# Performance work log

Measured on AMD Instinct MI355X. Metric: run time of the kernel, lower is better.

The kernel has to match this reference:

```python
import jax, jax.numpy as jnp
import numpy as np

HIDDEN = 768
VOCAB = 30522
PAD_IDX = 0


def setup_inputs() -> dict:
    key = jax.random.key(0)
    ks = jax.random.split(key, 12)
    B, J, X, D, V, K = 32, 4, 256, HIDDEN, VOCAB, 8
    s = 0.02
    return {
        "decoder_input": jax.random.normal(ks[0], (B, J, D), jnp.float32),
        "hidden": jax.random.normal(ks[1], (1, B, D), jnp.float32),
        "encoder_output": jax.random.normal(ks[2], (B, X, D), jnp.float32),
        "input_ids": jax.random.randint(ks[3], (B, X), 0, V),
        "max_len": K,
        "emb": jax.random.normal(ks[4], (V, D), jnp.float32) * s,
        "w_ih": jax.random.normal(ks[5], (3 * D, D), jnp.float32) * s,
        "w_hh": jax.random.normal(ks[6], (3 * D, D), jnp.float32) * s,
        "b_ih": jnp.zeros((3 * D,), jnp.float32),
        "b_hh": jnp.zeros((3 * D,), jnp.float32),
        "w_gen": jax.random.normal(ks[7], (1, 3 * D), jnp.float32) * s,
        "b_gen": jnp.zeros((1,), jnp.float32),
    }


def _gru_cell(x, h, w_ih, w_hh, b_ih, b_hh):
    # PyTorch GRUCell math. x,h: (B,D)
    gi = x @ w_ih.T + b_ih  # (B,3D)
    gh = h @ w_hh.T + b_hh
    i_r, i_z, i_n = jnp.split(gi, 3, axis=-1)
    h_r, h_z, h_n = jnp.split(gh, 3, axis=-1)
    r = jax.nn.sigmoid(i_r + h_r)
    z = jax.nn.sigmoid(i_z + h_z)
    n = jnp.tanh(i_n + r * h_n)
    return (1.0 - z) * n + z * h


def _decode(decoder_input, hidden, encoder_output, input_ids, max_len,
            emb, w_ih, w_hh, b_ih, b_hh, w_gen, b_gen):
    B = input_ids.shape[0]
    V = emb.shape[0]
    mask = input_ids == PAD_IDX  # (B,X)
    rows = jnp.arange(B)[:, None]
    h0 = hidden[0]  # (B,D)

    def step(carry, _):
        x, h = carry  # (B,D), (B,D)
        h = _gru_cell(x, h, w_ih, w_hh, b_ih, b_hh)
        # vocab distribution
        p_vcb = jax.nn.softmax(h @ emb.T, axis=-1)  # (B,V)
        # context attention
        attn_ctx = jnp.einsum("bxd,bd->bx", encoder_output, h)
        attn_ctx = jnp.where(mask, -1e9, attn_ctx)
        attn_ctx = jax.nn.softmax(attn_ctx, axis=-1)  # (B,X)
        context = jnp.einsum("bx,bxd->bd", attn_ctx, encoder_output)
        # pointer-generator gate
        p_gen = jax.nn.sigmoid(
            jnp.concatenate([h, x, context], axis=-1) @ w_gen.T + b_gen
        )  # (B,1)
        # scatter copy probs into vocab space
        p_ctx = jnp.zeros((B, V), attn_ctx.dtype).at[rows, input_ids].add(attn_ctx)
        p_svg = p_gen * p_vcb + (1.0 - p_gen) * p_ctx  # (B,V)
        x_next = emb[jnp.argmax(p_svg, axis=-1)]  # greedy next input (B,D)
        return (x_next, h), p_svg

    outs = []
    h = h0
    for j in range(decoder_input.shape[1]):  # small fixed J'
        (_, h), p = jax.lax.scan(step, (decoder_input[:, j, :], h), None,
                                 length=max_len)
        outs.append(jnp.transpose(p, (1, 0, 2)))  # (B,K,V)
    return jnp.stack(outs, axis=1)  # (B,J',K,V)


def reference(decoder_input, hidden, encoder_output, input_ids, max_len,
              emb, w_ih, w_hh, b_ih, b_hh, w_gen, b_gen):
    return _decode(decoder_input, hidden, encoder_output, input_ids, max_len,
                   emb, w_ih, w_hh, b_ih, b_hh, w_gen, b_gen)
```

## Files before the change

### kernel.cpp

```cpp
#include <hip/hip_runtime.h>
#include <hip/hip_bf16.h>

#define D 768
#define BB 32
#define XX 256
#define CH 3816
#define NLG 128

typedef __bf16 bf16x8 __attribute__((ext_vector_type(8)));
typedef float  f32x4  __attribute__((ext_vector_type(4)));

__global__ __launch_bounds__(256) void k_cvt(const float* __restrict__ src,
                                             __bf16* __restrict__ dst, int n8)
{
    int i = blockIdx.x * 256 + threadIdx.x;
    if (i < n8) {
        float4 f0 = *(const float4*)(src + (size_t)i * 8);
        float4 f1 = *(const float4*)(src + (size_t)i * 8 + 4);
        bf16x8 o;
        o[0] = (__bf16)f0.x; o[1] = (__bf16)f0.y; o[2] = (__bf16)f0.z; o[3] = (__bf16)f0.w;
        o[4] = (__bf16)f1.x; o[5] = (__bf16)f1.y; o[6] = (__bf16)f1.z; o[7] = (__bf16)f1.w;
        *(bf16x8*)(dst + (size_t)i * 8) = o;
    }
}

__global__ __launch_bounds__(256) void k_penc(
    const float* __restrict__ enc, const float* __restrict__ wgen,
    float* __restrict__ penc)
{
    const int t = threadIdx.x;
    const int b = blockIdx.x >> 2, c = blockIdx.x & 3;
    const int x0 = c * 64;
    const int l = t & 31;
    float4 wr[6];
    #pragma unroll
    for (int p = 0; p < 6; ++p)
        wr[p] = *(const float4*)(wgen + 1536 + l * 4 + p * 128);
    for (int g = 0; g < 8; ++g) {
        int x = x0 + g * 8 + (t >> 5);
        const float* er = enc + ((size_t)b * XX + x) * D + l * 4;
        float acc = 0.f;
        #pragma unroll
        for (int p = 0; p < 6; ++p) {
            float4 e = *(const float4*)(er + p * 128);
            acc += e.x * wr[p].x + e.y * wr[p].y + e.z * wr[p].z + e.w * wr[p].w;
        }
        #pragma unroll
        for (int m = 1; m <= 16; m <<= 1) acc += __shfl_xor(acc, m);
        if (l == 0) penc[b * XX + x] = acc;
    }
}

__global__ __launch_bounds__(256) void k_gates(
    const float* __restrict__ xbase, long xbstride,
    const unsigned long long* __restrict__ toks,
    const float* __restrict__ hin,
    const float* __restrict__ wih, const float* __restrict__ whh,
    float* __restrict__ gT)
{
    __shared__ __align__(16) float vec[BB][132];
    __shared__ int tokl[BB];
    const int t = threadIdx.x, bid = blockIdx.x;
    const int b = t & 31, rl = t >> 5;
    const int rglob = bid * 8 + rl;
    const bool isH = rglob >= 2304;
    const int row = isH ? rglob - 2304 : rglob;
    const float* w = (isH ? whh : wih) + (size_t)row * D;
    if (t < 32) tokl[t] = toks ? (int)(0xFFFFFFFFu - (unsigned)(toks[t] & 0xFFFFFFFFull)) : 0;

    float acc = 0.f;
    for (int c = 0; c < 6; ++c) {
        const int kc = c * 128;
        __syncthreads();
        for (int p = 0; p < 4; ++p) {
            int fid = t + 256 * p;
            int bb = fid >> 5, k4 = (fid & 31) * 4;
            const float* src;
            if (isH) src = hin + (size_t)bb * D;
            else     src = toks ? (xbase + (size_t)tokl[bb] * D)
                                : (xbase + (size_t)bb * xbstride);
            *(float4*)&vec[bb][k4] = *(const float4*)(src + kc + k4);
        }
        __syncthreads();
        #pragma unroll
        for (int k4 = 0; k4 < 128; k4 += 4) {
            float4 wv = *(const float4*)(w + kc + k4);
            float4 xv = *(const float4*)&vec[b][k4];
            acc += wv.x * xv.x + wv.y * xv.y + wv.z * xv.z + wv.w * xv.w;
        }
    }
    gT[(size_t)rglob * 32 + b] = acc;
}

__global__ __launch_bounds__(256) void k_comb(
    const float* __restrict__ gT,
    const float* __restrict__ bih, const float* __restrict__ bhh,
    const float* __restrict__ hin,
    const float* __restrict__ xbase, long xbstride,
    const unsigned long long* __restrict__ toks,
    const float* __restrict__ wgen,
    float* __restrict__ hout, __bf16* __restrict__ hbf,
    float* __restrict__ pgen_part,
    unsigned long long* __restrict__ argz)
{
    __shared__ float part[8][32];
    const int t = threadIdx.x, bid = blockIdx.x;
    const int b = t & 31, dl = t >> 5;
    const int d = bid * 8 + dl;
    if (bid == 0 && t < 32) argz[t] = 0ULL;
    float ir = gT[(size_t)d * 32 + b]            + bih[d];
    float iz = gT[(size_t)(768 + d) * 32 + b]    + bih[768 + d];
    float in_ = gT[(size_t)(1536 + d) * 32 + b]  + bih[1536 + d];
    float hr = gT[(size_t)(2304 + d) * 32 + b]   + bhh[d];
    float hz = gT[(size_t)(3072 + d) * 32 + b]   + bhh[768 + d];
    float hn = gT[(size_t)(3840 + d) * 32 + b]   + bhh[1536 + d];
    float r = 1.0f / (1.0f + expf(-(ir + hr)));
    float z = 1.0f / (1.0f + expf(-(iz + hz)));
    float n = tanhf(in_ + r * hn);
    float hold = hin[(size_t)b * D + d];
    float hv = (1.0f - z) * n + z * hold;
    hout[(size_t)b * D + d] = hv;
    hbf[(size_t)b * D + d] = (__bf16)hv;
    float xv;
    if (toks) {
        int tok = (int)(0xFFFFFFFFu - (unsigned)(toks[b] & 0xFFFFFFFFull));
        xv = xbase[(size_t)tok * D + d];
    } else {
        xv = xbase[(size_t)b * xbstride + d];
    }
    part[dl][b] = wgen[d] * hv + wgen[768 + d] * xv;
    __syncthreads();
    if (t < 32) {
        float s = 0.f;
        #pragma unroll
        for (int i = 0; i < 8; ++i) s += part[i][t];
        pgen_part[(size_t)t * 96 + bid] = s;
    }
}

__global__ __launch_bounds__(256) void k_mid(
    const float* __restrict__ hnew, const __bf16* __restrict__ hbf,
    const __bf16* __restrict__ embbf,
    const float* __restrict__ enc, const int* __restrict__ ids,
    float* __restrict__ out, long outoff, long JKV,
    float* __restrict__ dpartT, float* __restrict__ logitw,
    int V, int NVB)
{
    __shared__ float dsum[32];
    __shared__ float sh[64][33];
    const int t = threadIdx.x;
    const int bid = blockIdx.x;

    if (bid < NLG) {
        const int nb = bid;
        const int b = nb >> 2, c = nb & 3;
        const int x0 = c * 64;
        const int l = t & 31;
        float4 hr[6];
        #pragma unroll
        for (int p = 0; p < 6; ++p)
            hr[p] = *(const float4*)(hnew + (size_t)b * D + l * 4 + p * 128);
        #pragma unroll 4
        for (int g = 0; g < 8; ++g) {
            int x = x0 + g * 8 + (t >> 5);
            const float* er = enc + ((size_t)b * XX + x) * D + l * 4;
            float acc = 0.f;
            #pragma unroll
            for (int p = 0; p < 6; ++p) {
                float4 e = *(const float4*)(er + p * 128);
                acc += e.x * hr[p].x + e.y * hr[p].y + e.z * hr[p].z + e.w * hr[p].w;
            }
            #pragma unroll
            for (int m = 1; m <= 16; m <<= 1) acc += __shfl_xor(acc, m);
            if (l == 0) {
                int id = ids[b * XX + x];
                logitw[b * XX + x] = (id == 0) ? -1e9f : acc;
            }
        }
    } else {
        const int vb = bid - NLG;
        if (t < 32) dsum[t] = 0.f;
        __syncthreads();

        const int lane = t & 63, w = t >> 6;
        const int col = lane & 15;
        const int kq  = (lane >> 4) * 8;
        int vrow = vb * 64 + w * 16 + col;
        const bool ok = vrow < V;
        const int vl = ok ? vrow : V - 1;
        const __bf16* bp  = embbf + (size_t)vl * D + kq;
        const __bf16* ap0 = hbf + (size_t)col * D + kq;
        const __bf16* ap1 = hbf + (size_t)(col + 16) * D + kq;

        bf16x8 bv[24];
        #pragma unroll
        for (int i = 0; i < 24; ++i)
            bv[i] = *(const bf16x8*)(bp + i * 32);

        f32x4 c0 = {0.f, 0.f, 0.f, 0.f};
        f32x4 c1 = {0.f, 0.f, 0.f, 0.f};
        #pragma unroll
        for (int i = 0; i < 24; ++i) {
            bf16x8 a0 = *(const bf16x8*)(ap0 + i * 32);
            bf16x8 a1 = *(const bf16x8*)(ap1 + i * 32);
            c0 = __builtin_amdgcn_mfma_f32_16x16x32_bf16(a0, bv[i], c0, 0, 0, 0);
            c1 = __builtin_amdgcn_mfma_f32_16x16x32_bf16(a1, bv[i], c1, 0, 0, 0);
        }

        const int vloc = w * 16 + col;
        #pragma unroll
        for (int r = 0; r < 4; ++r) {
            int b0 = (lane >> 4) * 4 + r;
            float e0 = ok ? __expf(c0[r]) : 0.f;
            float e1 = ok ? __expf(c1[r]) : 0.f;
            sh[vloc][b0]      = e0;
            sh[vloc][b0 + 16] = e1;
            #pragma unroll
            for (int m = 1; m <= 8; m <<= 1) {
                e0 += __shfl_xor(e0, m);
                e1 += __shfl_xor(e1, m);
            }
            if (col == 0) {
                atomicAdd(&dsum[b0], e0);
                atomicAdd(&dsum[b0 + 16], e1);
            }
        }
        __syncthreads();
        if (t < 32) dpartT[(size_t)t * 512 + vb] = dsum[t];

        const int li = lane;
        const int vg = vb * 64 + li;
        if (vg < V) {
            #pragma unroll
            for (int i = 0; i < 8; ++i) {
                int bb2 = w * 8 + i;
                out[(size_t)bb2 * JKV + outoff + vg] = sh[li][bb2];
            }
        }
    }
}

__global__ __launch_bounds__(256) void k_fin(
    float* __restrict__ out, long outoff, long JKV,
    const float* __restrict__ dpartT, int npart,
    const float* __restrict__ logitw, const float* __restrict__ penc,
    const float* __restrict__ pgen_part, const float* __restrict__ bgen,
    const int* __restrict__ ids,
    unsigned long long* __restrict__ argz, int V)
{
    __shared__ float pctx[CH];
    __shared__ float red[256];
    __shared__ float aw[256];
    __shared__ unsigned long long wmax[4];
    const int t = threadIdx.x;
    const int b = blockIdx.x >> 3;
    const int c = blockIdx.x & 7;
    const int v0 = c * CH;

    float s = 0.f;
    for (int i = t; i < npart; i += 256) s += dpartT[(size_t)b * 512 + i];
    red[t] = s;
    __syncthreads();
    for (int st = 128; st > 0; st >>= 1) {
        if (t < st) red[t] += red[t + st];
        __syncthreads();
    }
    const float rd = 1.0f / red[0];
    __syncthreads();

    float l = logitw[b * XX + t];
    red[t] = l;
    __syncthreads();
    for (int st = 128; st > 0; st >>= 1) {
        if (t < st) red[t] = fmaxf(red[t], red[t + st]);
        __syncthreads();
    }
    float mx = red[0];
    __syncthreads();
    float e = expf(l - mx);
    red[t] = e;
    __syncthreads();
    for (int st = 128; st > 0; st >>= 1) {
        if (t < st) red[t] += red[t + st];
        __syncthreads();
    }
    float awv = e / red[0];
    aw[t] = awv;
    __syncthreads();

    float pv = awv * penc[b * XX + t] + ((t < 96) ? pgen_part[(size_t)b * 96 + t] : 0.f);
    red[t] = pv;
    __syncthreads();
    for (int st = 128; st > 0; st >>= 1) {
        if (t < st) red[t] += red[t + st];
        __syncthreads();
    }
    const float pg = 1.0f / (1.0f + expf(-(red[0] + bgen[0])));
    const float og = 1.0f - pg;

    for (int i = t; i < CH; i += 256) pctx[i] = 0.f;
    __syncthreads();
    {
        int id = ids[b * XX + t];
        int rel = id - v0;
        if ((unsigned)rel < (unsigned)CH) atomicAdd(&pctx[rel], aw[t]);
    }
    __syncthreads();

    unsigned long long pk = 0ULL;
    const int vend = (v0 + CH < V) ? CH : (V - v0);
    #pragma unroll
    for (int i = 0; i < 15; ++i) {
        int v = t + 256 * i;
        if (v < vend) {
            int vg = v0 + v;
            size_t o = (size_t)b * JKV + outoff + vg;
            float ev = out[o];
            float ps = pg * ev * rd + og * pctx[v];
            out[o] = ps;
            unsigned long long k2 = ((unsigned long long)__float_as_uint(ps) << 32)
                                  | (unsigned long long)(0xFFFFFFFFu - (unsigned)vg);
            if (k2 > pk) pk = k2;
        }
    }
    #pragma unroll
    for (int m = 1; m < 64; m <<= 1) {
        unsigned long long o2 = __shfl_xor(pk, m);
        if (o2 > pk) pk = o2;
    }
    if ((t & 63) == 0) wmax[t >> 6] = pk;
    __syncthreads();
    if (t == 0) {
        unsigned long long m0 = wmax[0];
        #pragma unroll
        for (int i2 = 1; i2 < 4; ++i2) if (wmax[i2] > m0) m0 = wmax[i2];
        atomicMax(&argz[b], m0);
    }
}

extern "C" void kernel_launch(void* const* d_in, const int* in_sizes, int n_in,
                              void* d_out, int out_size, void* d_ws, size_t ws_size,
                              hipStream_t stream)
{
    const float* dec  = (const float*)d_in[0];
    const float* hid  = (const float*)d_in[1];
    const float* enc  = (const float*)d_in[2];
    const int*   ids  = (const int*)d_in[3];
    const float* emb  = (const float*)d_in[5];
    const float* wih  = (const float*)d_in[6];
    const float* whh  = (const float*)d_in[7];
    const float* bih  = (const float*)d_in[8];
    const float* bhh  = (const float*)d_in[9];
    const float* wgen = (const float*)d_in[10];
    const float* bgen = (const float*)d_in[11];
    float* out = (float*)d_out;

    const int B = 32;
    const int J = in_sizes[0] / (B * D);
    const int V = in_sizes[5] / D;
    const int K = out_size / (B * J * V);
    const long JKV = (long)J * K * V;
    const int NVB = (V + 63) / 64;

    char* w = (char*)d_ws;
    unsigned long long* argpack = (unsigned long long*)w; w += 1024;
    float* gT        = (float*)w;  w += (size_t)4608 * 32 * 4;
    float* dpartT    = (float*)w;  w += (size_t)32 * 512 * 4;
    float* logitw    = (float*)w;  w += (size_t)B * XX * 4;
    float* penc      = (float*)w;  w += (size_t)B * XX * 4;
    float* pgen_part = (float*)w;  w += (size_t)B * 96 * 4;
    float* h0        = (float*)w;  w += (size_t)B * D * 4;
    float* h1        = (float*)w;  w += (size_t)B * D * 4;
    __bf16* hbf      = (__bf16*)w; w += (size_t)B * D * 2;
    __bf16* embbf    = (__bf16*)w; w += (size_t)V * D * 2;

    const int n8 = V * D / 8;
    k_cvt<<<dim3((n8 + 255) / 256), dim3(256), 0, stream>>>(emb, embbf, n8);
    k_penc<<<dim3(128), dim3(256), 0, stream>>>(enc, wgen, penc);

    int step = 0;
    for (int j = 0; j < J; ++j) {
        for (int kk = 0; kk < K; ++kk) {
            const int cur = step & 1;
            float* hout = (cur == 0) ? h0 : h1;
            const float* hin = (step == 0) ? hid : ((((step - 1) & 1) == 0) ? h0 : h1);
            const float* xbase;
            long xbs;
            const unsigned long long* toks;
            if (kk == 0) {
                xbase = dec + (size_t)j * D;
                xbs = (long)J * D;
                toks = nullptr;
            } else {
                xbase = emb;
                xbs = D;
                toks = argpack + ((step - 1) & 1) * 32;
            }
            unsigned long long* argz = argpack + cur * 32;
            const long outoff = (long)(j * K + kk) * V;

            k_gates<<<dim3(576), dim3(256), 0, stream>>>(
                xbase, xbs, toks, hin, wih, whh, gT);
            k_comb<<<dim3(96), dim3(256), 0, stream>>>(
                gT, bih, bhh, hin, xbase, xbs, toks, wgen, hout, hbf,
                pgen_part, argz);
            k_mid<<<dim3(NVB + NLG), dim3(256), 0, stream>>>(
                hout, hbf, embbf, enc, ids, out, outoff, JKV,
                dpartT, logitw, V, NVB);
            k_fin<<<dim3(256), dim3(256), 0, stream>>>(
                out, outoff, JKV, dpartT, NVB, logitw, penc, pgen_part,
                bgen, ids, argz, V);
            ++step;
        }
    }
}
```

Measured before the change: 2.333 ms.

## Fuse GRU gates with combine, and fuse vocab logits with finalize via grid barrier

The per-step pipeline drops from four kernels to two. The GRU gate matvecs and the gate nonlinearity are merged into one 96-block kernel, which removes the gT round trip. The attention logits, the vocab MFMA with exp, the softmax normalisation, the copy scatter, the output write and the argmax now all run in one persistent 256-block kernel. That kernel uses atomic-counter grid barriers, so the exp values stay in shared memory and the output is no longer re-read from global memory. The trade-offs: the grid barriers need all 256 blocks to be co-resident to avoid deadlock, the fused GRU kernel runs only 96 blocks, each reading six weight rows, and the counter arrays index by step and are sized for at most 32 steps.

```diff
diff --git a/kernel.cpp b/kernel.cpp
--- a/kernel.cpp
+++ b/kernel.cpp
@@ -2,18 +2,18 @@
 #include <hip/hip_bf16.h>
 
 #define D 768
-#define BB 32
 #define XX 256
-#define CH 3816
-#define NLG 128
 
 typedef __bf16 bf16x8 __attribute__((ext_vector_type(8)));
 typedef float  f32x4  __attribute__((ext_vector_type(4)));
+typedef unsigned long long ull;
 
 __global__ __launch_bounds__(256) void k_cvt(const float* __restrict__ src,
-                                             __bf16* __restrict__ dst, int n8)
+                                             __bf16* __restrict__ dst, int n8,
+                                             unsigned* __restrict__ cnt)
 {
     int i = blockIdx.x * 256 + threadIdx.x;
+    if (blockIdx.x == 0 && threadIdx.x < 64) cnt[threadIdx.x] = 0u;
     if (i < n8) {
         float4 f0 = *(const float4*)(src + (size_t)i * 8);
         float4 f1 = *(const float4*)(src + (size_t)i * 8 + 4);
@@ -51,84 +51,82 @@
     }
 }
 
-__global__ __launch_bounds__(256) void k_gates(
-    const float* __restrict__ xbase, long xbstride,
+__global__ __launch_bounds__(256) void k_gru(
+    const float* __restrict__ xbase, long xbs,
     const unsigned long long* __restrict__ toks,
     const float* __restrict__ hin,
     const float* __restrict__ wih, const float* __restrict__ whh,
-    float* __restrict__ gT)
+    const float* __restrict__ bih, const float* __restrict__ bhh,
+    const float* __restrict__ wgen,
+    float* __restrict__ hout, __bf16* __restrict__ hbf,
+    float* __restrict__ pgen_part)
 {
-    __shared__ __align__(16) float vec[BB][132];
-    __shared__ int tokl[BB];
+    __shared__ __align__(16) float xs[32][132];
+    __shared__ __align__(16) float hs[32][132];
+    __shared__ int tokl[32];
+    __shared__ float part[8][32];
     const int t = threadIdx.x, bid = blockIdx.x;
     const int b = t & 31, rl = t >> 5;
-    const int rglob = bid * 8 + rl;
-    const bool isH = rglob >= 2304;
-    const int row = isH ? rglob - 2304 : rglob;
-    const float* w = (isH ? whh : wih) + (size_t)row * D;
-    if (t < 32) tokl[t] = toks ? (int)(0xFFFFFFFFu - (unsigned)(toks[t] & 0xFFFFFFFFull)) : 0;
-
-    float acc = 0.f;
+    const int d = bid * 8 + rl;
+    if (t < 32)
+        tokl[t] = toks ? (int)(0xFFFFFFFFu - (unsigned)(toks[t] & 0xFFFFFFFFull)) : 0;
+
+    const float* w0 = wih + (size_t)d * D;
+    const float* w1 = wih + (size_t)(768 + d) * D;
+    const float* w2 = wih + (size_t)(1536 + d) * D;
+    const float* w3 = whh + (size_t)d * D;
+    const float* w4 = whh + (size_t)(768 + d) * D;
+    const float* w5 = whh + (size_t)(1536 + d) * D;
+
+    float aIR = 0.f, aIZ = 0.f, aIN = 0.f, aHR = 0.f, aHZ = 0.f, aHN = 0.f;
     for (int c = 0; c < 6; ++c) {
         const int kc = c * 128;
         __syncthreads();
         for (int p = 0; p < 4; ++p) {
             int fid = t + 256 * p;
             int bb = fid >> 5, k4 = (fid & 31) * 4;
-            const float* src;
-            if (isH) src = hin + (size_t)bb * D;
-            else     src = toks ? (xbase + (size_t)tokl[bb] * D)
-                                : (xbase + (size_t)bb * xbstride);
-            *(float4*)&vec[bb][k4] = *(const float4*)(src + kc + k4);
+            const float* sx = toks ? (xbase + (size_t)tokl[bb] * D)
+                                   : (xbase + (size_t)bb * xbs);
+            *(float4*)&xs[bb][k4] = *(const float4*)(sx + kc + k4);
+            *(float4*)&hs[bb][k4] = *(const float4*)(hin + (size_t)bb * D + kc + k4);
         }
         __syncthreads();
-        #pragma unroll
+        #pragma unroll 8
         for (int k4 = 0; k4 < 128; k4 += 4) {
-            float4 wv = *(const float4*)(w + kc + k4);
-            float4 xv = *(const float4*)&vec[b][k4];
-            acc += wv.x * xv.x + wv.y * xv.y + wv.z * xv.z + wv.w * xv.w;
-        }
-    }
-    gT[(size_t)rglob * 32 + b] = acc;
-}
-
-__global__ __launch_bounds__(256) void k_comb(
-    const float* __restrict__ gT,
-    const float* __restrict__ bih, const float* __restrict__ bhh,
-    const float* __restrict__ hin,
-    const float* __restrict__ xbase, long xbstride,
-    const unsigned long long* __restrict__ toks,
-    const float* __restrict__ wgen,
-    float* __restrict__ hout, __bf16* __restrict__ hbf,
-    float* __restrict__ pgen_part,
-    unsigned long long* __restrict__ argz)
-{
-    __shared__ float part[8][32];
-    const int t = threadIdx.x, bid = blockIdx.x;
-    const int b = t & 31, dl = t >> 5;
-    const int d = bid * 8 + dl;
-    if (bid == 0 && t < 32) argz[t] = 0ULL;
-    float ir = gT[(size_t)d * 32 + b]            + bih[d];
-    float iz = gT[(size_t)(768 + d) * 32 + b]    + bih[768 + d];
-    float in_ = gT[(size_t)(1536 + d) * 32 + b]  + bih[1536 + d];
-    float hr = gT[(size_t)(2304 + d) * 32 + b]   + bhh[d];
-    float hz = gT[(size_t)(3072 + d) * 32 + b]   + bhh[768 + d];
-    float hn = gT[(size_t)(3840 + d) * 32 + b]   + bhh[1536 + d];
+            float4 xv = *(const float4*)&xs[b][k4];
+            float4 hv = *(const float4*)&hs[b][k4];
+            float4 wv;
+            wv = *(const float4*)(w0 + kc + k4);
+            aIR += wv.x * xv.x + wv.y * xv.y + wv.z * xv.z + wv.w * xv.w;
+            wv = *(const float4*)(w1 + kc + k4);
+            aIZ += wv.x * xv.x + wv.y * xv.y + wv.z * xv.z + wv.w * xv.w;
+            wv = *(const float4*)(w2 + kc + k4);
+            aIN += wv.x * xv.x + wv.y * xv.y + wv.z * xv.z + wv.w * xv.w;
+            wv = *(const float4*)(w3 + kc + k4);
+            aHR += wv.x * hv.x + wv.y * hv.y + wv.z * hv.z + wv.w * hv.w;
+            wv = *(const float4*)(w4 + kc + k4);
+            aHZ += wv.x * hv.x + wv.y * hv.y + wv.z * hv.z + wv.w * hv.w;
+            wv = *(const float4*)(w5 + kc + k4);
+            aHN += wv.x * hv.x + wv.y * hv.y + wv.z * hv.z + wv.w * hv.w;
+        }
+    }
+    float ir = aIR + bih[d];
+    float iz = aIZ + bih[768 + d];
+    float in_ = aIN + bih[1536 + d];
+    float hr = aHR + bhh[d];
+    float hz = aHZ + bhh[768 + d];
+    float hn = aHN + bhh[1536 + d];
     float r = 1.0f / (1.0f + expf(-(ir + hr)));
     float z = 1.0f / (1.0f + expf(-(iz + hz)));
     float n = tanhf(in_ + r * hn);
     float hold = hin[(size_t)b * D + d];
-    float hv = (1.0f - z) * n + z * hold;
-    hout[(size_t)b * D + d] = hv;
-    hbf[(size_t)b * D + d] = (__bf16)hv;
-    float xv;
-    if (toks) {
-        int tok = (int)(0xFFFFFFFFu - (unsigned)(toks[b] & 0xFFFFFFFFull));
-        xv = xbase[(size_t)tok * D + d];
-    } else {
-        xv = xbase[(size_t)b * xbstride + d];
-    }
-    part[dl][b] = wgen[d] * hv + wgen[768 + d] * xv;
+    float hv2 = (1.0f - z) * n + z * hold;
+    hout[(size_t)b * D + d] = hv2;
+    hbf[(size_t)b * D + d] = (__bf16)hv2;
+    float xv2;
+    if (toks) xv2 = xbase[(size_t)tokl[b] * D + d];
+    else      xv2 = xbase[(size_t)b * xbs + d];
+    part[rl][b] = wgen[d] * hv2 + wgen[768 + d] * xv2;
     __syncthreads();
     if (t < 32) {
         float s = 0.f;
@@ -138,30 +136,34 @@
     }
 }
 
-__global__ __launch_bounds__(256) void k_mid(
+__global__ __launch_bounds__(256) void k_midfin(
     const float* __restrict__ hnew, const __bf16* __restrict__ hbf,
     const __bf16* __restrict__ embbf,
     const float* __restrict__ enc, const int* __restrict__ ids,
+    const float* __restrict__ penc, const float* __restrict__ pgen_part,
+    const float* __restrict__ bgen,
     float* __restrict__ out, long outoff, long JKV,
     float* __restrict__ dpartT, float* __restrict__ logitw,
-    int V, int NVB)
+    ull* __restrict__ wmaxArr, ull* __restrict__ argz,
+    unsigned* __restrict__ doneA, unsigned* __restrict__ doneB,
+    int V, int NT)
 {
+    __shared__ float shEx[128][33];
+    __shared__ float shP[128][33];
     __shared__ float dsum[32];
-    __shared__ float sh[64][33];
-    const int t = threadIdx.x;
-    const int bid = blockIdx.x;
-
-    if (bid < NLG) {
-        const int nb = bid;
-        const int b = nb >> 2, c = nb & 3;
-        const int x0 = c * 64;
+    __shared__ float pgL[32], rdL[32], ogL[32];
+    __shared__ ull redq[256];
+    const int t = threadIdx.x, bid = blockIdx.x;
+    const int NBLK = gridDim.x;
+
+    {
+        const int b = bid >> 3, x0 = (bid & 7) * 32;
         const int l = t & 31;
         float4 hr[6];
         #pragma unroll
         for (int p = 0; p < 6; ++p)
             hr[p] = *(const float4*)(hnew + (size_t)b * D + l * 4 + p * 128);
-        #pragma unroll 4
-        for (int g = 0; g < 8; ++g) {
+        for (int g = 0; g < 4; ++g) {
             int x = x0 + g * 8 + (t >> 5);
             const float* er = enc + ((size_t)b * XX + x) * D + l * 4;
             float acc = 0.f;
@@ -177,164 +179,183 @@
                 logitw[b * XX + x] = (id == 0) ? -1e9f : acc;
             }
         }
-    } else {
-        const int vb = bid - NLG;
-        if (t < 32) dsum[t] = 0.f;
-        __syncthreads();
-
-        const int lane = t & 63, w = t >> 6;
-        const int col = lane & 15;
-        const int kq  = (lane >> 4) * 8;
-        int vrow = vb * 64 + w * 16 + col;
-        const bool ok = vrow < V;
-        const int vl = ok ? vrow : V - 1;
-        const __bf16* bp  = embbf + (size_t)vl * D + kq;
-        const __bf16* ap0 = hbf + (size_t)col * D + kq;
-        const __bf16* ap1 = hbf + (size_t)(col + 16) * D + kq;
-
-        bf16x8 bv[24];
-        #pragma unroll
-        for (int i = 0; i < 24; ++i)
-            bv[i] = *(const bf16x8*)(bp + i * 32);
-
-        f32x4 c0 = {0.f, 0.f, 0.f, 0.f};
-        f32x4 c1 = {0.f, 0.f, 0.f, 0.f};
-        #pragma unroll
-        for (int i = 0; i < 24; ++i) {
-            bf16x8 a0 = *(const bf16x8*)(ap0 + i * 32);
-            bf16x8 a1 = *(const bf16x8*)(ap1 + i * 32);
-            c0 = __builtin_amdgcn_mfma_f32_16x16x32_bf16(a0, bv[i], c0, 0, 0, 0);
-            c1 = __builtin_amdgcn_mfma_f32_16x16x32_bf16(a1, bv[i], c1, 0, 0, 0);
-        }
-
-        const int vloc = w * 16 + col;
-        #pragma unroll
-        for (int r = 0; r < 4; ++r) {
-            int b0 = (lane >> 4) * 4 + r;
-            float e0 = ok ? __expf(c0[r]) : 0.f;
-            float e1 = ok ? __expf(c1[r]) : 0.f;
-            sh[vloc][b0]      = e0;
-            sh[vloc][b0 + 16] = e1;
+    }
+
+    if (t < 32) dsum[t] = 0.f;
+    for (int i = t; i < 128 * 33; i += 256) ((float*)shP)[i] = 0.f;
+    __syncthreads();
+
+    const int lane = t & 63, wv_ = t >> 6;
+    const int col = lane & 15;
+    const int kq  = (lane >> 4) * 8;
+    const __bf16* ap0 = hbf + (size_t)col * D + kq;
+    const __bf16* ap1 = hbf + (size_t)(col + 16) * D + kq;
+
+    #pragma unroll
+    for (int s2 = 0; s2 < 2; ++s2) {
+        const int vt = bid + s2 * NBLK;
+        if (vt < NT) {
+            const int vrow = vt * 64 + wv_ * 16 + col;
+            const bool ok = vrow < V;
+            const __bf16* bp = embbf + (size_t)(ok ? vrow : V - 1) * D + kq;
+            f32x4 c0 = {0.f, 0.f, 0.f, 0.f};
+            f32x4 c1 = {0.f, 0.f, 0.f, 0.f};
             #pragma unroll
-            for (int m = 1; m <= 8; m <<= 1) {
-                e0 += __shfl_xor(e0, m);
-                e1 += __shfl_xor(e1, m);
-            }
-            if (col == 0) {
-                atomicAdd(&dsum[b0], e0);
-                atomicAdd(&dsum[b0 + 16], e1);
-            }
-        }
-        __syncthreads();
-        if (t < 32) dpartT[(size_t)t * 512 + vb] = dsum[t];
-
-        const int li = lane;
-        const int vg = vb * 64 + li;
+            for (int hh = 0; hh < 2; ++hh) {
+                bf16x8 bv[12];
+                #pragma unroll
+                for (int i = 0; i < 12; ++i)
+                    bv[i] = *(const bf16x8*)(bp + hh * 384 + i * 32);
+                #pragma unroll
+                for (int i = 0; i < 12; ++i) {
+                    bf16x8 a0 = *(const bf16x8*)(ap0 + hh * 384 + i * 32);
+                    bf16x8 a1 = *(const bf16x8*)(ap1 + hh * 384 + i * 32);
+                    c0 = __builtin_amdgcn_mfma_f32_16x16x32_bf16(a0, bv[i], c0, 0, 0, 0);
+                    c1 = __builtin_amdgcn_mfma_f32_16x16x32_bf16(a1, bv[i], c1, 0, 0, 0);
+                }
+            }
+            const int vloc = s2 * 64 + wv_ * 16 + col;
+            #pragma unroll
+            for (int r = 0; r < 4; ++r) {
+                int b0 = (lane >> 4) * 4 + r;
+                float e0 = ok ? __expf(c0[r]) : 0.f;
+                float e1 = ok ? __expf(c1[r]) : 0.f;
+                shEx[vloc][b0]      = e0;
+                shEx[vloc][b0 + 16] = e1;
+                #pragma unroll
+                for (int m = 1; m <= 8; m <<= 1) {
+                    e0 += __shfl_xor(e0, m);
+                    e1 += __shfl_xor(e1, m);
+                }
+                if (col == 0) {
+                    atomicAdd(&dsum[b0], e0);
+                    atomicAdd(&dsum[b0 + 16], e1);
+                }
+            }
+        }
+    }
+    __syncthreads();
+    if (t < 32) dpartT[(size_t)t * 256 + bid] = dsum[t];
+
+    __threadfence();
+    __syncthreads();
+    if (t == 0) {
+        atomicAdd(doneA, 1u);
+        while (__hip_atomic_load(doneA, __ATOMIC_RELAXED, __HIP_MEMORY_SCOPE_AGENT)
+               < (unsigned)NBLK)
+            __builtin_amdgcn_s_sleep(8);
+        __threadfence();
+    }
+    __syncthreads();
+
+    const int bg = t >> 3, l8 = t & 7;
+    float s = 0.f;
+    for (int i = l8; i < 256; i += 8) s += dpartT[(size_t)bg * 256 + i];
+    s += __shfl_xor(s, 1); s += __shfl_xor(s, 2); s += __shfl_xor(s, 4);
+    const float rd = 1.0f / s;
+    float lgv[32];
+    #pragma unroll
+    for (int i = 0; i < 32; ++i) lgv[i] = logitw[bg * XX + l8 * 32 + i];
+    float mx = -1e30f;
+    #pragma unroll
+    for (int i = 0; i < 32; ++i) mx = fmaxf(mx, lgv[i]);
+    mx = fmaxf(mx, __shfl_xor(mx, 1));
+    mx = fmaxf(mx, __shfl_xor(mx, 2));
+    mx = fmaxf(mx, __shfl_xor(mx, 4));
+    float asum = 0.f;
+    #pragma unroll
+    for (int i = 0; i < 32; ++i) {
+        float e = expf(lgv[i] - mx);
+        lgv[i] = e;
+        asum += e;
+    }
+    asum += __shfl_xor(asum, 1); asum += __shfl_xor(asum, 2); asum += __shfl_xor(asum, 4);
+    const float ainv = 1.0f / asum;
+    float pv = 0.f;
+    #pragma unroll
+    for (int i = 0; i < 32; ++i)
+        pv += lgv[i] * ainv * penc[bg * XX + l8 * 32 + i];
+    for (int i = l8; i < 96; i += 8) pv += pgen_part[(size_t)bg * 96 + i];
+    pv += __shfl_xor(pv, 1); pv += __shfl_xor(pv, 2); pv += __shfl_xor(pv, 4);
+    const float pg = 1.0f / (1.0f + expf(-(pv + bgen[0])));
+    if (l8 == 0) { pgL[bg] = pg; rdL[bg] = rd; ogL[bg] = 1.0f - pg; }
+    const int base0 = bid * 64;
+    const int base1 = (bid + NBLK) * 64;
+    const bool has1 = (bid + NBLK) < NT;
+    #pragma unroll
+    for (int i = 0; i < 32; ++i) {
+        int x = l8 * 32 + i;
+        int id = ids[bg * XX + x];
+        float awv = lgv[i] * ainv;
+        int r0 = id - base0;
+        if ((unsigned)r0 < 64u) atomicAdd(&shP[r0][bg], awv);
+        if (has1) {
+            int r1 = id - base1;
+            if ((unsigned)r1 < 64u) atomicAdd(&shP[64 + r1][bg], awv);
+        }
+    }
+    __syncthreads();
+    ull pk[8];
+    #pragma unroll
+    for (int i = 0; i < 8; ++i) pk[i] = 0ULL;
+    {
+        int vg = base0 + lane;
+        #pragma unroll
+        for (int i = 0; i < 8; ++i) {
+            int bb = wv_ * 8 + i;
+            float ps = pgL[bb] * rdL[bb] * shEx[lane][bb] + ogL[bb] * shP[lane][bb];
+            out[(size_t)bb * JKV + outoff + vg] = ps;
+            ull k2 = ((ull)__float_as_uint(ps) << 32)
+                   | (ull)(0xFFFFFFFFu - (unsigned)vg);
+            if (k2 > pk[i]) pk[i] = k2;
+        }
+    }
+    if (has1) {
+        int vg = base1 + lane;
         if (vg < V) {
             #pragma unroll
             for (int i = 0; i < 8; ++i) {
-                int bb2 = w * 8 + i;
-                out[(size_t)bb2 * JKV + outoff + vg] = sh[li][bb2];
-            }
-        }
-    }
-}
-
-__global__ __launch_bounds__(256) void k_fin(
-    float* __restrict__ out, long outoff, long JKV,
-    const float* __restrict__ dpartT, int npart,
-    const float* __restrict__ logitw, const float* __restrict__ penc,
-    const float* __restrict__ pgen_part, const float* __restrict__ bgen,
-    const int* __restrict__ ids,
-    unsigned long long* __restrict__ argz, int V)
-{
-    __shared__ float pctx[CH];
-    __shared__ float red[256];
-    __shared__ float aw[256];
-    __shared__ unsigned long long wmax[4];
-    const int t = threadIdx.x;
-    const int b = blockIdx.x >> 3;
-    const int c = blockIdx.x & 7;
-    const int v0 = c * CH;
-
-    float s = 0.f;
-    for (int i = t; i < npart; i += 256) s += dpartT[(size_t)b * 512 + i];
-    red[t] = s;
-    __syncthreads();
-    for (int st = 128; st > 0; st >>= 1) {
-        if (t < st) red[t] += red[t + st];
+                int bb = wv_ * 8 + i;
+                float ps = pgL[bb] * rdL[bb] * shEx[64 + lane][bb] + ogL[bb] * shP[64 + lane][bb];
+                out[(size_t)bb * JKV + outoff + vg] = ps;
+                ull k2 = ((ull)__float_as_uint(ps) << 32)
+                       | (ull)(0xFFFFFFFFu - (unsigned)vg);
+                if (k2 > pk[i]) pk[i] = k2;
+            }
+        }
+    }
+    #pragma unroll
+    for (int i = 0; i < 8; ++i) {
+        #pragma unroll
+        for (int m = 1; m < 64; m <<= 1) {
+            ull o2 = __shfl_xor(pk[i], m);
+            if (o2 > pk[i]) pk[i] = o2;
+        }
+    }
+    if (lane == 0) {
+        #pragma unroll
+        for (int i = 0; i < 8; ++i)
+            wmaxArr[(size_t)bid * 32 + wv_ * 8 + i] = pk[i];
+    }
+    __threadfence();
+    __syncthreads();
+    if (t == 0) atomicAdd(doneB, 1u);
+
+    if (bid < 32) {
+        if (t == 0) {
+            while (__hip_atomic_load(doneB, __ATOMIC_RELAXED, __HIP_MEMORY_SCOPE_AGENT)
+                   < (unsigned)NBLK)
+                __builtin_amdgcn_s_sleep(8);
+            __threadfence();
+        }
         __syncthreads();
-    }
-    const float rd = 1.0f / red[0];
-    __syncthreads();
-
-    float l = logitw[b * XX + t];
-    red[t] = l;
-    __syncthreads();
-    for (int st = 128; st > 0; st >>= 1) {
-        if (t < st) red[t] = fmaxf(red[t], red[t + st]);
+        redq[t] = wmaxArr[(size_t)t * 32 + bid];
         __syncthreads();
-    }
-    float mx = red[0];
-    __syncthreads();
-    float e = expf(l - mx);
-    red[t] = e;
-    __syncthreads();
-    for (int st = 128; st > 0; st >>= 1) {
-        if (t < st) red[t] += red[t + st];
-        __syncthreads();
-    }
-    float awv = e / red[0];
-    aw[t] = awv;
-    __syncthreads();
-
-    float pv = awv * penc[b * XX + t] + ((t < 96) ? pgen_part[(size_t)b * 96 + t] : 0.f);
-    red[t] = pv;
-    __syncthreads();
-    for (int st = 128; st > 0; st >>= 1) {
-        if (t < st) red[t] += red[t + st];
-        __syncthreads();
-    }
-    const float pg = 1.0f / (1.0f + expf(-(red[0] + bgen[0])));
-    const float og = 1.0f - pg;
-
-    for (int i = t; i < CH; i += 256) pctx[i] = 0.f;
-    __syncthreads();
-    {
-        int id = ids[b * XX + t];
-        int rel = id - v0;
-        if ((unsigned)rel < (unsigned)CH) atomicAdd(&pctx[rel], aw[t]);
-    }
-    __syncthreads();
-
-    unsigned long long pk = 0ULL;
-    const int vend = (v0 + CH < V) ? CH : (V - v0);
-    #pragma unroll
-    for (int i = 0; i < 15; ++i) {
-        int v = t + 256 * i;
-        if (v < vend) {
-            int vg = v0 + v;
-            size_t o = (size_t)b * JKV + outoff + vg;
-            float ev = out[o];
-            float ps = pg * ev * rd + og * pctx[v];
-            out[o] = ps;
-            unsigned long long k2 = ((unsigned long long)__float_as_uint(ps) << 32)
-                                  | (unsigned long long)(0xFFFFFFFFu - (unsigned)vg);
-            if (k2 > pk) pk = k2;
-        }
-    }
-    #pragma unroll
-    for (int m = 1; m < 64; m <<= 1) {
-        unsigned long long o2 = __shfl_xor(pk, m);
-        if (o2 > pk) pk = o2;
-    }
-    if ((t & 63) == 0) wmax[t >> 6] = pk;
-    __syncthreads();
-    if (t == 0) {
-        unsigned long long m0 = wmax[0];
-        #pragma unroll
-        for (int i2 = 1; i2 < 4; ++i2) if (wmax[i2] > m0) m0 = wmax[i2];
-        atomicMax(&argz[b], m0);
+        for (int st = 128; st > 0; st >>= 1) {
+            if (t < st) { if (redq[t + st] > redq[t]) redq[t] = redq[t + st]; }
+            __syncthreads();
+        }
+        if (t == 0) argz[bid] = redq[0];
     }
 }
 
@@ -360,27 +381,28 @@
     const int V = in_sizes[5] / D;
     const int K = out_size / (B * J * V);
     const long JKV = (long)J * K * V;
-    const int NVB = (V + 63) / 64;
+    const int NT = (V + 63) / 64;
 
     char* w = (char*)d_ws;
-    unsigned long long* argpack = (unsigned long long*)w; w += 1024;
-    float* gT        = (float*)w;  w += (size_t)4608 * 32 * 4;
-    float* dpartT    = (float*)w;  w += (size_t)32 * 512 * 4;
-    float* logitw    = (float*)w;  w += (size_t)B * XX * 4;
-    float* penc      = (float*)w;  w += (size_t)B * XX * 4;
-    float* pgen_part = (float*)w;  w += (size_t)B * 96 * 4;
-    float* h0        = (float*)w;  w += (size_t)B * D * 4;
-    float* h1        = (float*)w;  w += (size_t)B * D * 4;
-    __bf16* hbf      = (__bf16*)w; w += (size_t)B * D * 2;
-    __bf16* embbf    = (__bf16*)w; w += (size_t)V * D * 2;
+    ull*  argpack   = (ull*)w;      w += 1024;
+    float* dpartT    = (float*)w;   w += (size_t)32 * 256 * 4;
+    float* logitw    = (float*)w;   w += (size_t)B * XX * 4;
+    float* penc      = (float*)w;   w += (size_t)B * XX * 4;
+    float* pgen_part = (float*)w;   w += (size_t)B * 96 * 4;
+    float* h0        = (float*)w;   w += (size_t)B * D * 4;
+    float* h1        = (float*)w;   w += (size_t)B * D * 4;
+    ull*  wmaxArr   = (ull*)w;      w += (size_t)256 * 32 * 8;
+    unsigned* cnt    = (unsigned*)w; w += 64 * 4;
+    __bf16* hbf      = (__bf16*)w;  w += (size_t)B * D * 2;
+    __bf16* embbf    = (__bf16*)w;  w += (size_t)V * D * 2;
 
     const int n8 = V * D / 8;
-    k_cvt<<<dim3((n8 + 255) / 256), dim3(256), 0, stream>>>(emb, embbf, n8);
+    k_cvt<<<dim3((n8 + 255) / 256), dim3(256), 0, stream>>>(emb, embbf, n8, cnt);
     k_penc<<<dim3(128), dim3(256), 0, stream>>>(enc, wgen, penc);
 
     int step = 0;
     for (int j = 0; j < J; ++j) {
-        for (int kk = 0; kk < K; ++kk) {
+        for (int kk = 0; kk < K; ++kk, ++step) {
             const int cur = step & 1;
             float* hout = (cur == 0) ? h0 : h1;
             const float* hin = (step == 0) ? hid : ((((step - 1) & 1) == 0) ? h0 : h1);
@@ -396,21 +418,16 @@
                 xbs = D;
                 toks = argpack + ((step - 1) & 1) * 32;
             }
-            unsigned long long* argz = argpack + cur * 32;
+            ull* argz = argpack + cur * 32;
             const long outoff = (long)(j * K + kk) * V;
 
-            k_gates<<<dim3(576), dim3(256), 0, stream>>>(
-                xbase, xbs, toks, hin, wih, whh, gT);
-            k_comb<<<dim3(96), dim3(256), 0, stream>>>(
-                gT, bih, bhh, hin, xbase, xbs, toks, wgen, hout, hbf,
-                pgen_part, argz);
-            k_mid<<<dim3(NVB + NLG), dim3(256), 0, stream>>>(
-                hout, hbf, embbf, enc, ids, out, outoff, JKV,
-                dpartT, logitw, V, NVB);
-            k_fin<<<dim3(256), dim3(256), 0, stream>>>(
-                out, outoff, JKV, dpartT, NVB, logitw, penc, pgen_part,
-                bgen, ids, argz, V);
-            ++step;
+            k_gru<<<dim3(96), dim3(256), 0, stream>>>(
+                xbase, xbs, toks, hin, wih, whh, bih, bhh, wgen,
+                hout, hbf, pgen_part);
+            k_midfin<<<dim3(256), dim3(256), 0, stream>>>(
+                hout, hbf, embbf, enc, ids, penc, pgen_part, bgen,
+                out, outoff, JKV, dpartT, logitw, wmaxArr, argz,
+                cnt + step, cnt + 32 + step, V, NT);
         }
     }
 }
```

After: 4.956 ms. 112% more time.

## Stream embedding tiles into LDS with async double-buffered global_load_lds

Applied to the files above, without the earlier changes.

The vocab-logit blocks in k_mid no longer load each embedding row's full 768-wide slice into 24 registers up front. They now stream 128-column chunks into a double-buffered, XOR-swizzled LDS tile with global_load_lds, overlapping the next chunk's load with MFMAs on the current one. The LDS buffer is shared through a union with the softmax scratch arrays, which are re-zeroed after the GEMM loop. This aims to cut register pressure and hide memory latency on the bandwidth-heavy embedding stream. In exchange it adds manual vmcnt waits and LDS traffic, and relies on each wave reading only the rows it staged itself.

```diff
diff --git a/kernel.cpp b/kernel.cpp
--- a/kernel.cpp
+++ b/kernel.cpp
@@ -138,6 +138,28 @@
     }
 }
 
+struct __align__(16) MSE { float sh[64][33]; float dsum[32]; };
+union  __align__(16) MSU { __bf16 buf[2][64][128]; MSE e; };
+
+__device__ __forceinline__ void stage_chunk(
+    const char* __restrict__ embb, int vb, int c, int w, int lane,
+    char* lbuf, int V)
+{
+    #pragma unroll
+    for (int i = 0; i < 4; ++i) {
+        const int g = w * 4 + i;
+        const int row = g * 4 + (lane >> 4);
+        int grow = vb * 64 + row;
+        grow = (grow < V) ? grow : (V - 1);
+        const int cb = ((lane & 15) << 4) ^ ((row & 7) << 4);
+        const char* gp = embb + (size_t)grow * 1536 + (size_t)c * 256 + cb;
+        char* lp = lbuf + g * 1024;
+        __builtin_amdgcn_global_load_lds(
+            (const __attribute__((address_space(1))) unsigned int*)gp,
+            (__attribute__((address_space(3))) unsigned int*)lp, 16, 0, 0);
+    }
+}
+
 __global__ __launch_bounds__(256) void k_mid(
     const float* __restrict__ hnew, const __bf16* __restrict__ hbf,
     const __bf16* __restrict__ embbf,
@@ -146,14 +168,12 @@
     float* __restrict__ dpartT, float* __restrict__ logitw,
     int V, int NVB)
 {
-    __shared__ float dsum[32];
-    __shared__ float sh[64][33];
+    __shared__ MSU u;
     const int t = threadIdx.x;
     const int bid = blockIdx.x;
 
     if (bid < NLG) {
-        const int nb = bid;
-        const int b = nb >> 2, c = nb & 3;
+        const int b = bid >> 2, c = bid & 3;
         const int x0 = c * 64;
         const int l = t & 31;
         float4 hr[6];
@@ -179,62 +199,72 @@
         }
     } else {
         const int vb = bid - NLG;
-        if (t < 32) dsum[t] = 0.f;
-        __syncthreads();
-
         const int lane = t & 63, w = t >> 6;
         const int col = lane & 15;
-        const int kq  = (lane >> 4) * 8;
-        int vrow = vb * 64 + w * 16 + col;
+        const int hi = lane >> 4;
+        const int vrow = vb * 64 + w * 16 + col;
         const bool ok = vrow < V;
-        const int vl = ok ? vrow : V - 1;
-        const __bf16* bp  = embbf + (size_t)vl * D + kq;
-        const __bf16* ap0 = hbf + (size_t)col * D + kq;
-        const __bf16* ap1 = hbf + (size_t)(col + 16) * D + kq;
-
-        bf16x8 bv[24];
-        #pragma unroll
-        for (int i = 0; i < 24; ++i)
-            bv[i] = *(const bf16x8*)(bp + i * 32);
+        const __bf16* ap0 = hbf + (size_t)col * D + hi * 8;
+        const __bf16* ap1 = hbf + (size_t)(col + 16) * D + hi * 8;
+        const char* embb = (const char*)embbf;
+
+        stage_chunk(embb, vb, 0, w, lane, (char*)&u.buf[0][0][0], V);
 
         f32x4 c0 = {0.f, 0.f, 0.f, 0.f};
         f32x4 c1 = {0.f, 0.f, 0.f, 0.f};
-        #pragma unroll
-        for (int i = 0; i < 24; ++i) {
-            bf16x8 a0 = *(const bf16x8*)(ap0 + i * 32);
-            bf16x8 a1 = *(const bf16x8*)(ap1 + i * 32);
-            c0 = __builtin_amdgcn_mfma_f32_16x16x32_bf16(a0, bv[i], c0, 0, 0, 0);
-            c1 = __builtin_amdgcn_mfma_f32_16x16x32_bf16(a1, bv[i], c1, 0, 0, 0);
-        }
-
+        const int rl = w * 16 + col;
+        const int swz = (rl & 7) << 4;
+        for (int c = 0; c < 6; ++c) {
+            if (c < 5) {
+                stage_chunk(embb, vb, c + 1, w, lane,
+                            (char*)&u.buf[(c + 1) & 1][0][0], V);
+                asm volatile("s_waitcnt vmcnt(4)" ::: "memory");
+            } else {
+                asm volatile("s_waitcnt vmcnt(0)" ::: "memory");
+            }
+            const char* bbuf = (const char*)&u.buf[c & 1][0][0];
+            #pragma unroll
+            for (int q = 0; q < 4; ++q) {
+                const int cbl = q * 64 + (hi << 4);
+                bf16x8 bv = *(const bf16x8*)(bbuf + rl * 256 + (cbl ^ swz));
+                const int kg = c * 128 + q * 32;
+                bf16x8 a0 = *(const bf16x8*)(ap0 + kg);
+                bf16x8 a1 = *(const bf16x8*)(ap1 + kg);
+                c0 = __builtin_amdgcn_mfma_f32_16x16x32_bf16(a0, bv, c0, 0, 0, 0);
+                c1 = __builtin_amdgcn_mfma_f32_16x16x32_bf16(a1, bv, c1, 0, 0, 0);
+            }
+        }
+
+        __syncthreads();
+        if (t < 32) u.e.dsum[t] = 0.f;
+        __syncthreads();
         const int vloc = w * 16 + col;
         #pragma unroll
         for (int r = 0; r < 4; ++r) {
-            int b0 = (lane >> 4) * 4 + r;
+            int b0 = hi * 4 + r;
             float e0 = ok ? __expf(c0[r]) : 0.f;
             float e1 = ok ? __expf(c1[r]) : 0.f;
-            sh[vloc][b0]      = e0;
-            sh[vloc][b0 + 16] = e1;
+            u.e.sh[vloc][b0]      = e0;
+            u.e.sh[vloc][b0 + 16] = e1;
             #pragma unroll
             for (int m = 1; m <= 8; m <<= 1) {
                 e0 += __shfl_xor(e0, m);
                 e1 += __shfl_xor(e1, m);
             }
             if (col == 0) {
-                atomicAdd(&dsum[b0], e0);
-                atomicAdd(&dsum[b0 + 16], e1);
-            }
-        }
-        __syncthreads();
-        if (t < 32) dpartT[(size_t)t * 512 + vb] = dsum[t];
-
-        const int li = lane;
-        const int vg = vb * 64 + li;
+                atomicAdd(&u.e.dsum[b0], e0);
+                atomicAdd(&u.e.dsum[b0 + 16], e1);
+            }
+        }
+        __syncthreads();
+        if (t < 32) dpartT[(size_t)t * 512 + vb] = u.e.dsum[t];
+
+        const int vg = vb * 64 + lane;
         if (vg < V) {
             #pragma unroll
             for (int i = 0; i < 8; ++i) {
                 int bb2 = w * 8 + i;
-                out[(size_t)bb2 * JKV + outoff + vg] = sh[li][bb2];
+                out[(size_t)bb2 * JKV + outoff + vg] = u.e.sh[lane][bb2];
             }
         }
     }
```

Result: no change. 2.291 ms (-1.8%).
